# Optimization experiments

Measured on AMD Instinct MI355X. Metric: run time of the kernel, lower is better.

The kernel has to match this reference:

```python
import jax, jax.numpy as jnp
import numpy as np

NUM_HEADS = 5
TEMP = 0.3
NEG_FILL = -1e-7  # note: NOT -inf; masked entries still contribute ~exp(0) to softmax, faithful to torch code


def setup_inputs() -> dict:
    key = jax.random.key(0)
    k1, k2, k3, k4, k5 = jax.random.split(key, 5)
    B, N, F_IN, F_OUT = 8, 1024, 320, 320
    h = jax.random.normal(k1, (B, N, F_IN), dtype=jnp.float32)
    Wqk = jax.random.normal(k2, (F_IN, 2 * F_IN), dtype=jnp.float32) * (1.0 / np.sqrt(F_IN))
    bqk = jax.random.normal(k3, (2 * F_IN,), dtype=jnp.float32) * 0.01
    weight = jax.random.normal(k4, (F_IN, F_OUT), dtype=jnp.float32) * (1.0 / np.sqrt(F_OUT))
    bias = jax.random.normal(k5, (F_OUT,), dtype=jnp.float32) * 0.01
    return {"h": h, "Wqk": Wqk, "bqk": bqk, "weight": weight, "bias": bias}


def reference(h, Wqk, bqk, weight, bias):
    B, N, F = h.shape
    H = NUM_HEADS
    D = F // H
    # linear -> [b, n, 2F]; einops 'b n (h d qk)' => reshape (b, n, h, d, 2)
    qk = (h @ Wqk + bqk).reshape(B, N, H, D, 2)
    q = jnp.transpose(qk[..., 0], (0, 2, 1, 3))  # b h n d
    k = jnp.transpose(qk[..., 1], (0, 2, 1, 3))  # b h n d
    scale = D ** -0.5
    dots = jnp.einsum('bhqd,bhkd->bhqk', q, k) * scale  # b h n n
    at = dots.sum(axis=1)  # b n n  (sum over heads)
    # sort-based threshold: keep values >= descending-sorted value at index N//6
    thr = jax.lax.top_k(at, N // 6 + 1)[0][..., -1]  # b n
    adj = jnp.where(at < thr[:, :, None], jnp.asarray(NEG_FILL, at.dtype), at)
    attn = jax.nn.softmax(adj / TEMP, axis=2)  # b n n
    out_feature = jnp.einsum('bij,bjd->bid', attn, h)  # values = raw input h
    return out_feature @ weight + bias
```

## Files before the change

kernel.cpp:

```cpp
#include <hip/hip_runtime.h>
#include <hip/hip_fp16.h>


typedef __attribute__((ext_vector_type(8))) _Float16 half8;
typedef __attribute__((ext_vector_type(4))) float f32x4;

__device__ __forceinline__ void stage_tile(const __half* g, __half* lds,
                                           int nrow16, int ld, int wave, int lane) {
    const int r = lane >> 2;
    const int c = ((lane & 3) ^ ((lane >> 3) & 3)) * 8;
    for (int i = wave; i < nrow16; i += 4) {
        const __half* src = g + (long)(i * 16 + r) * ld + c;
        __builtin_amdgcn_global_load_lds(
            (const __attribute__((address_space(1))) unsigned int*)src,
            (__attribute__((address_space(3))) unsigned int*)(lds + i * 512),
            16, 0, 0);
    }
}

template <int WM, int WN, int EPI, int CH>
__global__ __launch_bounds__(256) void gemm_nt(
    const __half* __restrict__ A, const __half* __restrict__ B,
    void* __restrict__ C, void* __restrict__ C2,
    const float* __restrict__ bias,
    int K, int lda, int ldb, int ldc,
    long sA, long sB, long sC, float alpha)
{
    constexpr int BM = WM * 64;
    constexpr int BN = WN * 64;
    constexpr int A_EL = BM * 32;
    constexpr int B_EL = BN * 32;
    constexpr int BUF = (A_EL + B_EL) * CH;
    __shared__ __half smem[2 * BUF];

    const int tid  = threadIdx.x;
    const int lane = tid & 63;
    const int wave = tid >> 6;
    const int wm   = wave / WN;
    const int wn   = wave % WN;
    const int bz   = blockIdx.z;

    const __half* Ab = A + bz * sA + (long)blockIdx.y * BM * lda;
    const __half* Bb = B + bz * sB + (long)blockIdx.x * BN * ldb;

    f32x4 acc[4][4];
    #pragma unroll
    for (int i = 0; i < 4; ++i)
        #pragma unroll
        for (int j = 0; j < 4; ++j) acc[i][j] = (f32x4){0.f, 0.f, 0.f, 0.f};

    const int lrow = lane & 15;
    const int quad = lane >> 4;
    const int swz = (quad ^ ((lrow >> 1) & 3)) * 8;

    const int nIter = K / (32 * CH);

    #pragma unroll
    for (int c = 0; c < CH; ++c) {
        stage_tile(Ab + c * 32, smem + c * A_EL, BM / 16, lda, wave, lane);
        stage_tile(Bb + c * 32, smem + CH * A_EL + c * B_EL, BN / 16, ldb, wave, lane);
    }

    for (int it = 0; it < nIter; ++it) {
        __syncthreads();
        if (it + 1 < nIter) {
            __half* nb = smem + ((it + 1) & 1) * BUF;
            const int k1 = (it + 1) * 32 * CH;
            #pragma unroll
            for (int c = 0; c < CH; ++c) {
                stage_tile(Ab + k1 + c * 32, nb + c * A_EL, BM / 16, lda, wave, lane);
                stage_tile(Bb + k1 + c * 32, nb + CH * A_EL + c * B_EL, BN / 16, ldb, wave, lane);
            }
        }
        const __half* buf = smem + (it & 1) * BUF;
        #pragma unroll
        for (int c = 0; c < CH; ++c) {
            const __half* pA = buf + c * A_EL + (wm * 64 + lrow) * 32 + swz;
            const __half* pB = buf + CH * A_EL + c * B_EL + (wn * 64 + lrow) * 32 + swz;
            half8 ah[4], bh[4];
            #pragma unroll
            for (int mt = 0; mt < 4; ++mt) ah[mt] = *(const half8*)(pA + mt * 512);
            #pragma unroll
            for (int nt = 0; nt < 4; ++nt) bh[nt] = *(const half8*)(pB + nt * 512);
            #pragma unroll
            for (int mt = 0; mt < 4; ++mt)
                #pragma unroll
                for (int nt = 0; nt < 4; ++nt)
                    acc[mt][nt] = __builtin_amdgcn_mfma_f32_16x16x32_f16(
                        ah[mt], bh[nt], acc[mt][nt], 0, 0, 0);
        }
    }

    const int row_base = blockIdx.y * BM + wm * 64;
    const int col_base = blockIdx.x * BN + wn * 64;
    #pragma unroll
    for (int mt = 0; mt < 4; ++mt)
        #pragma unroll
        for (int nt = 0; nt < 4; ++nt)
            #pragma unroll
            for (int r = 0; r < 4; ++r) {
                const int row = row_base + mt * 16 + quad * 4 + r;
                const int col = col_base + nt * 16 + lrow;
                const float v = acc[mt][nt][r];
                if (EPI == 1) {
                    const float val = v + bias[col];
                    const long idx = (long)row * 320 + (col >> 1);
                    if (col & 1) ((__half*)C2)[idx] = __float2half(val);
                    else         ((__half*)C)[idx]  = __float2half(val);
                } else if (EPI == 2) {
                    ((__half*)C)[(long)row * ldc + col] = __float2half(v);
                } else if (EPI == 3) {
                    ((float*)C)[bz * sC + (long)row * ldc + col] = v + bias[col];
                } else {
                    ((__half*)C)[bz * sC + (long)row * ldc + col] =
                        __float2half(alpha * v);
                }
            }
}

template <int EPI>
__device__ __forceinline__ void gemm_body(
    const __half* __restrict__ A, const __half* __restrict__ B,
    void* __restrict__ C, void* __restrict__ C2, const float* __restrict__ bias,
    int lda, int ldb, int ldc, int bx, int by, __half* smem)
{
    constexpr int BUF = 16384;
    const int tid  = threadIdx.x;
    const int lane = tid & 63;
    const int wave = tid >> 6;
    const int wm   = wave >> 1;
    const int wn   = wave & 1;

    const __half* Ab = A + (long)by * 128 * lda;
    const __half* Bb = B + (long)bx * 128 * ldb;

    f32x4 acc[4][4];
    #pragma unroll
    for (int i = 0; i < 4; ++i)
        #pragma unroll
        for (int j = 0; j < 4; ++j) acc[i][j] = (f32x4){0.f, 0.f, 0.f, 0.f};

    const int lrow = lane & 15;
    const int quad = lane >> 4;
    const int swz = (quad ^ ((lrow >> 1) & 3)) * 8;

    #pragma unroll
    for (int c = 0; c < 2; ++c) {
        stage_tile(Ab + c * 32, smem + c * 4096, 8, lda, wave, lane);
        stage_tile(Bb + c * 32, smem + 8192 + c * 4096, 8, ldb, wave, lane);
    }

    for (int it = 0; it < 5; ++it) {
        __syncthreads();
        if (it + 1 < 5) {
            __half* nb = smem + ((it + 1) & 1) * BUF;
            const int k1 = (it + 1) * 64;
            #pragma unroll
            for (int c = 0; c < 2; ++c) {
                stage_tile(Ab + k1 + c * 32, nb + c * 4096, 8, lda, wave, lane);
                stage_tile(Bb + k1 + c * 32, nb + 8192 + c * 4096, 8, ldb, wave, lane);
            }
        }
        const __half* buf = smem + (it & 1) * BUF;
        #pragma unroll
        for (int c = 0; c < 2; ++c) {
            const __half* pA = buf + c * 4096 + (wm * 64 + lrow) * 32 + swz;
            const __half* pB = buf + 8192 + c * 4096 + (wn * 64 + lrow) * 32 + swz;
            half8 ah[4], bh[4];
            #pragma unroll
            for (int mt = 0; mt < 4; ++mt) ah[mt] = *(const half8*)(pA + mt * 512);
            #pragma unroll
            for (int nt = 0; nt < 4; ++nt) bh[nt] = *(const half8*)(pB + nt * 512);
            #pragma unroll
            for (int mt = 0; mt < 4; ++mt)
                #pragma unroll
                for (int nt = 0; nt < 4; ++nt)
                    acc[mt][nt] = __builtin_amdgcn_mfma_f32_16x16x32_f16(
                        ah[mt], bh[nt], acc[mt][nt], 0, 0, 0);
        }
    }

    const int row_base = by * 128 + wm * 64;
    const int col_base = bx * 128 + wn * 64;
    #pragma unroll
    for (int mt = 0; mt < 4; ++mt)
        #pragma unroll
        for (int nt = 0; nt < 4; ++nt)
            #pragma unroll
            for (int r = 0; r < 4; ++r) {
                const int row = row_base + mt * 16 + quad * 4 + r;
                const int col = col_base + nt * 16 + lrow;
                const float v = acc[mt][nt][r];
                if (EPI == 1) {
                    const float val = v + bias[col];
                    const long idx = (long)row * 320 + (col >> 1);
                    if (col & 1) ((__half*)C2)[idx] = __float2half(val);
                    else         ((__half*)C)[idx]  = __float2half(val);
                } else {
                    ((__half*)C)[(long)row * ldc + col] = __float2half(v);
                }
            }
}

__global__ __launch_bounds__(256) void g1_combined(
    const __half* __restrict__ h16, const __half* __restrict__ wTp,
    const __half* __restrict__ WqkT, __half* __restrict__ hWT,
    __half* __restrict__ Q, __half* __restrict__ Kb,
    const float* __restrict__ bqk)
{
    __shared__ __half smem[2 * 16384];
    const int bx = blockIdx.x;
    if (bx < 192) {
        gemm_body<2>(wTp, h16, hWT, nullptr, nullptr,
                     320, 320, 8192, bx % 64, bx / 64, smem);
    } else {
        const int b = bx - 192;
        gemm_body<1>(h16, WqkT, Q, Kb, bqk,
                     320, 320, 320, b % 5, b / 5, smem);
    }
}

__global__ __launch_bounds__(256) void prep_all(
    const float* __restrict__ h, ushort4* __restrict__ h16,
    const float* __restrict__ Wqk, __half* __restrict__ WqkT,
    const float* __restrict__ weight, __half* __restrict__ wTp)
{
    const int bx = blockIdx.x;
    if (bx < 2560) {
        const int i = bx * 256 + threadIdx.x;
        const float4 v = ((const float4*)h)[i];
        ushort4 o;
        o.x = __half_as_ushort(__float2half(v.x));
        o.y = __half_as_ushort(__float2half(v.y));
        o.z = __half_as_ushort(__float2half(v.z));
        o.w = __half_as_ushort(__float2half(v.w));
        h16[i] = o;
        return;
    }
    __shared__ float t[32][33];
    const float* src;
    __half* dst;
    int ldS, ldT, c0, r0;
    if (bx < 2760) {
        const int b = bx - 2560;
        src = Wqk; dst = WqkT; ldS = 640; ldT = 320;
        c0 = (b % 20) * 32; r0 = (b / 20) * 32;
    } else {
        const int b = bx - 2760;
        src = weight; dst = wTp; ldS = 320; ldT = 320;
        c0 = (b % 10) * 32; r0 = (b / 10) * 32;
    }
    const int lx = threadIdx.x & 31, ly = threadIdx.x >> 5;
    #pragma unroll
    for (int i = 0; i < 4; ++i)
        t[ly + 8 * i][lx] = src[(long)(r0 + ly + 8 * i) * ldS + c0 + lx];
    __syncthreads();
    #pragma unroll
    for (int i = 0; i < 4; ++i)
        dst[(long)(c0 + ly + 8 * i) * ldT + r0 + lx] = __float2half(t[lx][ly + 8 * i]);
}

__global__ __launch_bounds__(256) void topk_softmax(const __half* __restrict__ at,
                                                    __half* __restrict__ attn)
{
    __shared__ int hist[4][256];
    const int lane = threadIdx.x & 63;
    const int wave = threadIdx.x >> 6;
    const long row = (long)blockIdx.x * 4 + wave;

    unsigned short vs[16];
    {
        const uint4* p = (const uint4*)(at + row * 1024 + lane * 16);
        *(uint4*)&vs[0] = p[0];
        *(uint4*)&vs[8] = p[1];
    }

    unsigned key[16];
    #pragma unroll
    for (int i = 0; i < 16; ++i) {
        const unsigned u = vs[i];
        key[i] = (u & 0x8000u) ? ((~u) & 0xFFFFu) : (u | 0x8000u);
    }

    unsigned prefix = 0, pmask = 0;
    int kk = 171;

    #pragma unroll
    for (int pass = 0; pass < 2; ++pass) {
        const int shift = 8 - 8 * pass;
        *(int4*)&hist[wave][lane * 4] = make_int4(0, 0, 0, 0);
        __syncthreads();
        #pragma unroll
        for (int i = 0; i < 16; ++i) {
            if ((key[i] & pmask) == prefix)
                atomicAdd(&hist[wave][(key[i] >> shift) & 255], 1);
        }
        __syncthreads();
        const int4 hh = *(const int4*)&hist[wave][lane * 4];
        const int s = hh.x + hh.y + hh.z + hh.w;
        int suf = s;
        #pragma unroll
        for (int off = 1; off < 64; off <<= 1) {
            const int o = __shfl_down(suf, off);
            if (lane + off < 64) suf += o;
        }
        const int cgt3 = suf - s;
        const int cgt2 = cgt3 + hh.w;
        const int cgt1 = cgt2 + hh.z;
        const int cgt0 = cgt1 + hh.y;
        int pick = 0x7FFFFFFF;
        if (cgt3 < kk && kk <= cgt3 + hh.w) pick = ((4 * lane + 3) << 16) | (kk - cgt3);
        if (cgt2 < kk && kk <= cgt2 + hh.z) pick = ((4 * lane + 2) << 16) | (kk - cgt2);
        if (cgt1 < kk && kk <= cgt1 + hh.y) pick = ((4 * lane + 1) << 16) | (kk - cgt1);
        if (cgt0 < kk && kk <= cgt0 + hh.x) pick = ((4 * lane + 0) << 16) | (kk - cgt0);
        #pragma unroll
        for (int off = 32; off > 0; off >>= 1) pick = min(pick, __shfl_xor(pick, off));
        const unsigned digit = (unsigned)(pick >> 16);
        kk = pick & 0xFFFF;
        prefix |= digit << shift;
        pmask  |= 0xFFu << shift;
        if (pass == 0) __syncthreads();
    }

    const unsigned short tu = (prefix & 0x8000u) ? (unsigned short)(prefix & 0x7FFFu)
                                                 : (unsigned short)((~prefix) & 0xFFFFu);
    const float thr = __half2float(__ushort_as_half(tu));

    float lg[16];
    float mx = -3.4e38f;
    #pragma unroll
    for (int i = 0; i < 16; ++i) {
        const float v = __half2float(__ushort_as_half(vs[i]));
        const float a = (v < thr) ? -1e-7f : v;
        lg[i] = a * (1.0f / 0.3f);
        mx = fmaxf(mx, lg[i]);
    }
    #pragma unroll
    for (int off = 32; off > 0; off >>= 1) mx = fmaxf(mx, __shfl_xor(mx, off));

    float e[16];
    float sum = 0.f;
    #pragma unroll
    for (int i = 0; i < 16; ++i) { e[i] = __expf(lg[i] - mx); sum += e[i]; }
    #pragma unroll
    for (int off = 32; off > 0; off >>= 1) sum += __shfl_xor(sum, off);
    const float inv = 1.0f / sum;

    unsigned short os[16];
    #pragma unroll
    for (int i = 0; i < 16; ++i) os[i] = __half_as_ushort(__float2half(e[i] * inv));
    uint4* q = (uint4*)(attn + row * 1024 + lane * 16);
    q[0] = *(const uint4*)&os[0];
    q[1] = *(const uint4*)&os[8];
}

extern "C" void kernel_launch(void* const* d_in, const int* in_sizes, int n_in,
                              void* d_out, int out_size, void* d_ws, size_t ws_size,
                              hipStream_t stream) {
    (void)in_sizes; (void)n_in; (void)out_size; (void)ws_size;

    const float* h      = (const float*)d_in[0];
    const float* Wqk    = (const float*)d_in[1];
    const float* bqk    = (const float*)d_in[2];
    const float* weight = (const float*)d_in[3];
    const float* bias   = (const float*)d_in[4];
    float* out = (float*)d_out;

    char* p = (char*)d_ws;
    __half* at   = (__half*)p; p += 8388608L * 2;
    __half* attn = (__half*)p; p += 8388608L * 2;
    __half* h16  = (__half*)p; p += 2621440L * 2;
    __half* Q    = (__half*)p; p += 2621440L * 2;
    __half* Kb   = (__half*)p; p += 2621440L * 2;
    __half* WqkT = (__half*)p; p += 640L * 320 * 2;
    __half* wTp  = (__half*)p; p += 384L * 320 * 2;
    __half* hWT  = (__half*)p; p += 384L * 8192 * 2;

    prep_all<<<2860, 256, 0, stream>>>(h, (ushort4*)h16, Wqk, WqkT, weight, wTp);

    g1_combined<<<512, 256, 0, stream>>>(h16, wTp, WqkT, hWT, Q, Kb, bqk);

    gemm_nt<2, 2, 4, 2><<<dim3(8, 8, 8), 256, 0, stream>>>(
        Q, Kb, at, nullptr, nullptr,
        320, 320, 320, 1024, 327680, 327680, 1048576, 0.125f);

    topk_softmax<<<2048, 256, 0, stream>>>(at, attn);

    gemm_nt<4, 1, 3, 2><<<dim3(5, 4, 8), 256, 0, stream>>>(
        attn, hWT, out, nullptr, bias,
        1024, 1024, 8192, 320, 1048576, 1024, 327680, 1.0f);
}
```

Measured before the change: 132.1 us.

## Fuse QK^T, top-k threshold softmax, and PV GEMM into one kernel

Replaces the three kernels (scores GEMM, top-k/softmax, attention-times-values GEMM) with a single 512-thread kernel. Each block computes a 32-row strip of scores into an XOR-swizzled LDS buffer, runs the radix-select threshold and softmax in place, then multiplies by the values with a split-K reduction through LDS. This removes the global round trips of the two 16 MB fp16 score and attention matrices and two kernel launches. The cost is only 256 blocks with large LDS use, so occupancy and parallelism are lower, and each block re-reads all of K for its batch.

Result: slower. 137.2 us (+3.8%).

```diff
diff --git a/kernel.cpp b/kernel.cpp
--- a/kernel.cpp
+++ b/kernel.cpp
@@ -18,104 +18,17 @@
     }
 }
 
-template <int WM, int WN, int EPI, int CH>
-__global__ __launch_bounds__(256) void gemm_nt(
-    const __half* __restrict__ A, const __half* __restrict__ B,
-    void* __restrict__ C, void* __restrict__ C2,
-    const float* __restrict__ bias,
-    int K, int lda, int ldb, int ldc,
-    long sA, long sB, long sC, float alpha)
-{
-    constexpr int BM = WM * 64;
-    constexpr int BN = WN * 64;
-    constexpr int A_EL = BM * 32;
-    constexpr int B_EL = BN * 32;
-    constexpr int BUF = (A_EL + B_EL) * CH;
-    __shared__ __half smem[2 * BUF];
-
-    const int tid  = threadIdx.x;
-    const int lane = tid & 63;
-    const int wave = tid >> 6;
-    const int wm   = wave / WN;
-    const int wn   = wave % WN;
-    const int bz   = blockIdx.z;
-
-    const __half* Ab = A + bz * sA + (long)blockIdx.y * BM * lda;
-    const __half* Bb = B + bz * sB + (long)blockIdx.x * BN * ldb;
-
-    f32x4 acc[4][4];
-    #pragma unroll
-    for (int i = 0; i < 4; ++i)
-        #pragma unroll
-        for (int j = 0; j < 4; ++j) acc[i][j] = (f32x4){0.f, 0.f, 0.f, 0.f};
-
-    const int lrow = lane & 15;
-    const int quad = lane >> 4;
-    const int swz = (quad ^ ((lrow >> 1) & 3)) * 8;
-
-    const int nIter = K / (32 * CH);
-
-    #pragma unroll
-    for (int c = 0; c < CH; ++c) {
-        stage_tile(Ab + c * 32, smem + c * A_EL, BM / 16, lda, wave, lane);
-        stage_tile(Bb + c * 32, smem + CH * A_EL + c * B_EL, BN / 16, ldb, wave, lane);
-    }
-
-    for (int it = 0; it < nIter; ++it) {
-        __syncthreads();
-        if (it + 1 < nIter) {
-            __half* nb = smem + ((it + 1) & 1) * BUF;
-            const int k1 = (it + 1) * 32 * CH;
-            #pragma unroll
-            for (int c = 0; c < CH; ++c) {
-                stage_tile(Ab + k1 + c * 32, nb + c * A_EL, BM / 16, lda, wave, lane);
-                stage_tile(Bb + k1 + c * 32, nb + CH * A_EL + c * B_EL, BN / 16, ldb, wave, lane);
-            }
-        }
-        const __half* buf = smem + (it & 1) * BUF;
-        #pragma unroll
-        for (int c = 0; c < CH; ++c) {
-            const __half* pA = buf + c * A_EL + (wm * 64 + lrow) * 32 + swz;
-            const __half* pB = buf + CH * A_EL + c * B_EL + (wn * 64 + lrow) * 32 + swz;
-            half8 ah[4], bh[4];
-            #pragma unroll
-            for (int mt = 0; mt < 4; ++mt) ah[mt] = *(const half8*)(pA + mt * 512);
-            #pragma unroll
-            for (int nt = 0; nt < 4; ++nt) bh[nt] = *(const half8*)(pB + nt * 512);
-            #pragma unroll
-            for (int mt = 0; mt < 4; ++mt)
-                #pragma unroll
-                for (int nt = 0; nt < 4; ++nt)
-                    acc[mt][nt] = __builtin_amdgcn_mfma_f32_16x16x32_f16(
-                        ah[mt], bh[nt], acc[mt][nt], 0, 0, 0);
-        }
-    }
-
-    const int row_base = blockIdx.y * BM + wm * 64;
-    const int col_base = blockIdx.x * BN + wn * 64;
-    #pragma unroll
-    for (int mt = 0; mt < 4; ++mt)
-        #pragma unroll
-        for (int nt = 0; nt < 4; ++nt)
-            #pragma unroll
-            for (int r = 0; r < 4; ++r) {
-                const int row = row_base + mt * 16 + quad * 4 + r;
-                const int col = col_base + nt * 16 + lrow;
-                const float v = acc[mt][nt][r];
-                if (EPI == 1) {
-                    const float val = v + bias[col];
-                    const long idx = (long)row * 320 + (col >> 1);
-                    if (col & 1) ((__half*)C2)[idx] = __float2half(val);
-                    else         ((__half*)C)[idx]  = __float2half(val);
-                } else if (EPI == 2) {
-                    ((__half*)C)[(long)row * ldc + col] = __float2half(v);
-                } else if (EPI == 3) {
-                    ((float*)C)[bz * sC + (long)row * ldc + col] = v + bias[col];
-                } else {
-                    ((__half*)C)[bz * sC + (long)row * ldc + col] =
-                        __float2half(alpha * v);
-                }
-            }
+__device__ __forceinline__ void stage_tile8(const __half* g, __half* lds,
+                                            int nrow16, int ld, int wave, int lane) {
+    const int r = lane >> 2;
+    const int c = ((lane & 3) ^ ((lane >> 3) & 3)) * 8;
+    for (int i = wave; i < nrow16; i += 8) {
+        const __half* src = g + (long)(i * 16 + r) * ld + c;
+        __builtin_amdgcn_global_load_lds(
+            (const __attribute__((address_space(1))) unsigned int*)src,
+            (__attribute__((address_space(3))) unsigned int*)(lds + i * 512),
+            16, 0, 0);
+    }
 }
 
 template <int EPI>
@@ -260,98 +173,238 @@
         dst[(long)(c0 + ly + 8 * i) * ldT + r0 + lx] = __float2half(t[lx][ly + 8 * i]);
 }
 
-__global__ __launch_bounds__(256) void topk_softmax(const __half* __restrict__ at,
-                                                    __half* __restrict__ attn)
+__global__ __launch_bounds__(512, 2) void fused_attn(
+    const __half* __restrict__ Q, const __half* __restrict__ Kmat,
+    const __half* __restrict__ hWT, const float* __restrict__ bias,
+    float* __restrict__ out)
 {
-    __shared__ int hist[4][256];
-    const int lane = threadIdx.x & 63;
-    const int wave = threadIdx.x >> 6;
-    const long row = (long)blockIdx.x * 4 + wave;
-
-    unsigned short vs[16];
-    {
-        const uint4* p = (const uint4*)(at + row * 1024 + lane * 16);
-        *(uint4*)&vs[0] = p[0];
-        *(uint4*)&vs[8] = p[1];
-    }
-
-    unsigned key[16];
-    #pragma unroll
-    for (int i = 0; i < 16; ++i) {
-        const unsigned u = vs[i];
-        key[i] = (u & 0x8000u) ? ((~u) & 0xFFFFu) : (u | 0x8000u);
-    }
-
-    unsigned prefix = 0, pmask = 0;
-    int kk = 171;
-
-    #pragma unroll
-    for (int pass = 0; pass < 2; ++pass) {
-        const int shift = 8 - 8 * pass;
-        *(int4*)&hist[wave][lane * 4] = make_int4(0, 0, 0, 0);
+    __shared__ __half smem[75776];
+    __half* const P = smem;
+    __half* const X = smem + 32768;
+
+    const int tid  = threadIdx.x;
+    const int lane = tid & 63;
+    const int wave = tid >> 6;
+    const int lrow = lane & 15;
+    const int quad = lane >> 4;
+    const int swz  = (quad ^ ((lrow >> 1) & 3)) * 8;
+
+    const int b  = blockIdx.x & 7;
+    const int r0 = (blockIdx.x >> 3) * 32;
+
+    const __half* Qb = Q    + (long)(b * 1024 + r0) * 320;
+    const __half* Kb = Kmat + (long)b * 327680;
+    const __half* Wb = hWT  + (long)b * 1024;
+
+    __half* const Xq = X;
+    __half* const XB = X + 10240;
+
+    #pragma unroll
+    for (int c = 0; c < 10; ++c)
+        stage_tile8(Qb + c * 32, Xq + c * 1024, 2, 320, wave, lane);
+    stage_tile8(Kb, XB, 32, 320, wave, lane);
+
+    f32x4 acc[2][4];
+    #pragma unroll
+    for (int i = 0; i < 2; ++i)
+        #pragma unroll
+        for (int j = 0; j < 4; ++j) acc[i][j] = (f32x4){0.f, 0.f, 0.f, 0.f};
+
+    for (int r = 0; r < 20; ++r) {
         __syncthreads();
+        if (r + 1 < 20) {
+            const int rn = r + 1;
+            stage_tile8(Kb + (long)(rn / 10) * 512 * 320 + (rn % 10) * 32,
+                        XB + (rn & 1) * 16384, 32, 320, wave, lane);
+        }
+        const int ks = r % 10;
+        const __half* Bt = XB + (r & 1) * 16384;
+        const __half* At = Xq + ks * 1024;
+        half8 ah[2], bh[4];
+        #pragma unroll
+        for (int mi = 0; mi < 2; ++mi)
+            ah[mi] = *(const half8*)(At + (mi * 16 + lrow) * 32 + swz);
+        #pragma unroll
+        for (int nf = 0; nf < 4; ++nf)
+            bh[nf] = *(const half8*)(Bt + (wave * 64 + nf * 16 + lrow) * 32 + swz);
+        #pragma unroll
+        for (int mi = 0; mi < 2; ++mi)
+            #pragma unroll
+            for (int nf = 0; nf < 4; ++nf)
+                acc[mi][nf] = __builtin_amdgcn_mfma_f32_16x16x32_f16(
+                    ah[mi], bh[nf], acc[mi][nf], 0, 0, 0);
+        if (ks == 9) {
+            const int cb = (r / 10) * 512 + wave * 64;
+            #pragma unroll
+            for (int mi = 0; mi < 2; ++mi)
+                #pragma unroll
+                for (int nf = 0; nf < 4; ++nf)
+                    #pragma unroll
+                    for (int rr = 0; rr < 4; ++rr) {
+                        const int row = mi * 16 + quad * 4 + rr;
+                        const int col = cb + nf * 16 + lrow;
+                        P[((row << 10) + col) ^ ((row & 7) << 3)] =
+                            __float2half(0.125f * acc[mi][nf][rr]);
+                        acc[mi][nf][rr] = 0.f;
+                    }
+        }
+    }
+
+    __syncthreads();
+    stage_tile8(Wb,       X,         20, 8192, wave, lane);
+    stage_tile8(Wb + 512, X + 20480, 20, 8192, wave, lane);
+
+    int (*const hist)[256] = (int(*)[256])(X + 10240);
+
+    for (int j = 0; j < 4; ++j) {
+        const int row  = wave * 4 + j;
+        const int key8 = (row & 7) << 3;
+        const int base = (row << 10) + lane * 16;
+
+        unsigned short vs[16];
+        *(uint4*)&vs[0] = *(const uint4*)&P[base ^ key8];
+        *(uint4*)&vs[8] = *(const uint4*)&P[(base + 8) ^ key8];
+
+        unsigned key[16];
         #pragma unroll
         for (int i = 0; i < 16; ++i) {
-            if ((key[i] & pmask) == prefix)
-                atomicAdd(&hist[wave][(key[i] >> shift) & 255], 1);
-        }
+            const unsigned u = vs[i];
+            key[i] = (u & 0x8000u) ? ((~u) & 0xFFFFu) : (u | 0x8000u);
+        }
+
+        unsigned prefix = 0, pmask = 0;
+        int kk = 171;
+
+        #pragma unroll
+        for (int pass = 0; pass < 2; ++pass) {
+            const int shift = 8 - 8 * pass;
+            *(int4*)&hist[wave][lane * 4] = make_int4(0, 0, 0, 0);
+            __syncthreads();
+            #pragma unroll
+            for (int i = 0; i < 16; ++i) {
+                if ((key[i] & pmask) == prefix)
+                    atomicAdd(&hist[wave][(key[i] >> shift) & 255], 1);
+            }
+            __syncthreads();
+            const int4 hh = *(const int4*)&hist[wave][lane * 4];
+            const int s = hh.x + hh.y + hh.z + hh.w;
+            int suf = s;
+            #pragma unroll
+            for (int off = 1; off < 64; off <<= 1) {
+                const int o = __shfl_down(suf, off);
+                if (lane + off < 64) suf += o;
+            }
+            const int cgt3 = suf - s;
+            const int cgt2 = cgt3 + hh.w;
+            const int cgt1 = cgt2 + hh.z;
+            const int cgt0 = cgt1 + hh.y;
+            int pick = 0x7FFFFFFF;
+            if (cgt3 < kk && kk <= cgt3 + hh.w) pick = ((4 * lane + 3) << 16) | (kk - cgt3);
+            if (cgt2 < kk && kk <= cgt2 + hh.z) pick = ((4 * lane + 2) << 16) | (kk - cgt2);
+            if (cgt1 < kk && kk <= cgt1 + hh.y) pick = ((4 * lane + 1) << 16) | (kk - cgt1);
+            if (cgt0 < kk && kk <= cgt0 + hh.x) pick = ((4 * lane + 0) << 16) | (kk - cgt0);
+            #pragma unroll
+            for (int off = 32; off > 0; off >>= 1) pick = min(pick, __shfl_xor(pick, off));
+            const unsigned digit = (unsigned)(pick >> 16);
+            kk = pick & 0xFFFF;
+            prefix |= digit << shift;
+            pmask  |= 0xFFu << shift;
+            if (pass == 0) __syncthreads();
+        }
+
+        const unsigned short tu = (prefix & 0x8000u) ? (unsigned short)(prefix & 0x7FFFu)
+                                                     : (unsigned short)((~prefix) & 0xFFFFu);
+        const float thr = __half2float(__ushort_as_half(tu));
+
+        float lg[16];
+        float mx = -3.4e38f;
+        #pragma unroll
+        for (int i = 0; i < 16; ++i) {
+            const float v = __half2float(__ushort_as_half(vs[i]));
+            const float a = (v < thr) ? -1e-7f : v;
+            lg[i] = a * (1.0f / 0.3f);
+            mx = fmaxf(mx, lg[i]);
+        }
+        #pragma unroll
+        for (int off = 32; off > 0; off >>= 1) mx = fmaxf(mx, __shfl_xor(mx, off));
+
+        float e[16];
+        float sum = 0.f;
+        #pragma unroll
+        for (int i = 0; i < 16; ++i) { e[i] = __expf(lg[i] - mx); sum += e[i]; }
+        #pragma unroll
+        for (int off = 32; off > 0; off >>= 1) sum += __shfl_xor(sum, off);
+        const float inv = 1.0f / sum;
+
+        unsigned short os[16];
+        #pragma unroll
+        for (int i = 0; i < 16; ++i) os[i] = __half_as_ushort(__float2half(e[i] * inv));
+        *(uint4*)&P[base ^ key8]       = *(const uint4*)&os[0];
+        *(uint4*)&P[(base + 8) ^ key8] = *(const uint4*)&os[8];
+    }
+
+    const int q4 = wave & 3;
+    const int kh = wave >> 2;
+
+    f32x4 acc4[2][5];
+    #pragma unroll
+    for (int i = 0; i < 2; ++i)
+        #pragma unroll
+        for (int j = 0; j < 5; ++j) acc4[i][j] = (f32x4){0.f, 0.f, 0.f, 0.f};
+
+    for (int r = 0; r < 16; ++r) {
         __syncthreads();
-        const int4 hh = *(const int4*)&hist[wave][lane * 4];
-        const int s = hh.x + hh.y + hh.z + hh.w;
-        int suf = s;
-        #pragma unroll
-        for (int off = 1; off < 64; off <<= 1) {
-            const int o = __shfl_down(suf, off);
-            if (lane + off < 64) suf += o;
-        }
-        const int cgt3 = suf - s;
-        const int cgt2 = cgt3 + hh.w;
-        const int cgt1 = cgt2 + hh.z;
-        const int cgt0 = cgt1 + hh.y;
-        int pick = 0x7FFFFFFF;
-        if (cgt3 < kk && kk <= cgt3 + hh.w) pick = ((4 * lane + 3) << 16) | (kk - cgt3);
-        if (cgt2 < kk && kk <= cgt2 + hh.z) pick = ((4 * lane + 2) << 16) | (kk - cgt2);
-        if (cgt1 < kk && kk <= cgt1 + hh.y) pick = ((4 * lane + 1) << 16) | (kk - cgt1);
-        if (cgt0 < kk && kk <= cgt0 + hh.x) pick = ((4 * lane + 0) << 16) | (kk - cgt0);
-        #pragma unroll
-        for (int off = 32; off > 0; off >>= 1) pick = min(pick, __shfl_xor(pick, off));
-        const unsigned digit = (unsigned)(pick >> 16);
-        kk = pick & 0xFFFF;
-        prefix |= digit << shift;
-        pmask  |= 0xFFu << shift;
-        if (pass == 0) __syncthreads();
-    }
-
-    const unsigned short tu = (prefix & 0x8000u) ? (unsigned short)(prefix & 0x7FFFu)
-                                                 : (unsigned short)((~prefix) & 0xFFFFu);
-    const float thr = __half2float(__ushort_as_half(tu));
-
-    float lg[16];
-    float mx = -3.4e38f;
-    #pragma unroll
-    for (int i = 0; i < 16; ++i) {
-        const float v = __half2float(__ushort_as_half(vs[i]));
-        const float a = (v < thr) ? -1e-7f : v;
-        lg[i] = a * (1.0f / 0.3f);
-        mx = fmaxf(mx, lg[i]);
-    }
-    #pragma unroll
-    for (int off = 32; off > 0; off >>= 1) mx = fmaxf(mx, __shfl_xor(mx, off));
-
-    float e[16];
-    float sum = 0.f;
-    #pragma unroll
-    for (int i = 0; i < 16; ++i) { e[i] = __expf(lg[i] - mx); sum += e[i]; }
-    #pragma unroll
-    for (int off = 32; off > 0; off >>= 1) sum += __shfl_xor(sum, off);
-    const float inv = 1.0f / sum;
-
-    unsigned short os[16];
-    #pragma unroll
-    for (int i = 0; i < 16; ++i) os[i] = __half_as_ushort(__float2half(e[i] * inv));
-    uint4* q = (uint4*)(attn + row * 1024 + lane * 16);
-    q[0] = *(const uint4*)&os[0];
-    q[1] = *(const uint4*)&os[8];
+        if (r + 1 < 16) {
+            stage_tile8(Wb + (r + 1) * 32,       X + ((r + 1) & 1) * 10240,
+                        20, 8192, wave, lane);
+            stage_tile8(Wb + 512 + (r + 1) * 32, X + 20480 + ((r + 1) & 1) * 10240,
+                        20, 8192, wave, lane);
+        }
+        const __half* T = X + kh * 20480 + (r & 1) * 10240;
+        const int kk = kh * 512 + r * 32 + quad * 8;
+        half8 ah[2], bh[5];
+        #pragma unroll
+        for (int mi = 0; mi < 2; ++mi) {
+            const int row = mi * 16 + lrow;
+            ah[mi] = *(const half8*)&P[((row << 10) + kk) ^ ((row & 7) << 3)];
+        }
+        #pragma unroll
+        for (int nf = 0; nf < 5; ++nf)
+            bh[nf] = *(const half8*)(T + (q4 * 80 + nf * 16 + lrow) * 32 + swz);
+        #pragma unroll
+        for (int mi = 0; mi < 2; ++mi)
+            #pragma unroll
+            for (int nf = 0; nf < 5; ++nf)
+                acc4[mi][nf] = __builtin_amdgcn_mfma_f32_16x16x32_f16(
+                    ah[mi], bh[nf], acc4[mi][nf], 0, 0, 0);
+    }
+
+    __syncthreads();
+    float* const red = (float*)X;
+    if (kh == 1) {
+        #pragma unroll
+        for (int mi = 0; mi < 2; ++mi)
+            #pragma unroll
+            for (int nf = 0; nf < 5; ++nf)
+                #pragma unroll
+                for (int rr = 0; rr < 4; ++rr)
+                    red[(mi * 16 + quad * 4 + rr) * 320 + q4 * 80 + nf * 16 + lrow] =
+                        acc4[mi][nf][rr];
+    }
+    __syncthreads();
+    if (kh == 0) {
+        #pragma unroll
+        for (int mi = 0; mi < 2; ++mi)
+            #pragma unroll
+            for (int nf = 0; nf < 5; ++nf)
+                #pragma unroll
+                for (int rr = 0; rr < 4; ++rr) {
+                    const int row = mi * 16 + quad * 4 + rr;
+                    const int col = q4 * 80 + nf * 16 + lrow;
+                    out[(long)(b * 1024 + r0 + row) * 320 + col] =
+                        acc4[mi][nf][rr] + red[row * 320 + col] + bias[col];
+                }
+    }
 }
 
 extern "C" void kernel_launch(void* const* d_in, const int* in_sizes, int n_in,
@@ -367,8 +420,6 @@
     float* out = (float*)d_out;
 
     char* p = (char*)d_ws;
-    __half* at   = (__half*)p; p += 8388608L * 2;
-    __half* attn = (__half*)p; p += 8388608L * 2;
     __half* h16  = (__half*)p; p += 2621440L * 2;
     __half* Q    = (__half*)p; p += 2621440L * 2;
     __half* Kb   = (__half*)p; p += 2621440L * 2;
@@ -380,13 +431,5 @@
 
     g1_combined<<<512, 256, 0, stream>>>(h16, wTp, WqkT, hWT, Q, Kb, bqk);
 
-    gemm_nt<2, 2, 4, 2><<<dim3(8, 8, 8), 256, 0, stream>>>(
-        Q, Kb, at, nullptr, nullptr,
-        320, 320, 320, 1024, 327680, 327680, 1048576, 0.125f);
-
-    topk_softmax<<<2048, 256, 0, stream>>>(at, attn);
-
-    gemm_nt<4, 1, 3, 2><<<dim3(5, 4, 8), 256, 0, stream>>>(
-        attn, hWT, out, nullptr, bias,
-        1024, 1024, 8192, 320, 1048576, 1024, 327680, 1.0f);
-}
+    fused_attn<<<256, 512, 0, stream>>>(Q, Kb, hWT, bias, out);
+}
```
